# Performance work log

Hardware: AMD Instinct MI355X
Metric: run time of the kernel (lower is better)

The kernel has to match this reference:

```python
import jax, jax.numpy as jnp
import numpy as np

T, H, I, E, Z, TOPK = 1024, 1024, 512, 32, 8, 4
ROUTED_SCALING = 1.0


def setup_inputs() -> dict:
    key = jax.random.key(0)
    k1, k2, k3, k4 = jax.random.split(key, 4)
    return {
        "hidden_states": jax.random.normal(k1, (T, H), jnp.float32),
        "router_w": jax.random.normal(k2, (E + Z, H), jnp.float32) * 0.02,
        "correction_bias": jnp.zeros((E + Z,), jnp.float32),
        "w_gate_up": jax.random.normal(k3, (E, 2 * I, H), jnp.float32) * 0.02,
        "w_down": jax.random.normal(k4, (E, H, I), jnp.float32) * 0.02,
        "top_k": TOPK,
    }


def reference(hidden_states, router_w, correction_bias, w_gate_up, w_down, top_k):
    # hidden_states: [T, H]; router_w: [E+Z, H]; w_gate_up: [E, 2I, H]; w_down: [E, H, I]
    t, h = hidden_states.shape
    e = w_gate_up.shape[0]
    i = w_down.shape[2]
    # --- router (float32, no bias; correction bias only affects selection) ---
    logits = jnp.einsum("th,eh->te", hidden_states.astype(jnp.float32), router_w)
    scores = jax.nn.softmax(logits, axis=-1)                     # [T, E+Z]
    _, idx = jax.lax.top_k(scores + correction_bias[None, :], top_k)  # [T, k]
    w = jnp.take_along_axis(scores, idx, axis=1) * ROUTED_SCALING     # renormalize=False
    # combine matrix [T, E+Z] (sparse top-k scattered dense)
    comb = jnp.zeros((t, scores.shape[1]), jnp.float32)
    comb = comb.at[jnp.arange(t)[:, None], idx].add(w)
    comb_routed = comb[:, :e].astype(hidden_states.dtype)        # [T, E]
    zero_w = comb[:, e:].sum(-1).astype(hidden_states.dtype)     # [T] identity zero-experts
    # --- grouped SiLU-gated expert MLPs (dense all-experts reference) ---
    gu = jnp.einsum("th,eih->eti", hidden_states, w_gate_up)     # [E, T, 2I]
    hmid = jax.nn.silu(gu[..., :i]) * gu[..., i:]                # [E, T, I]
    ye = jnp.einsum("eti,ehi->eth", hmid, w_down)                # [E, T, H]
    out = jnp.einsum("te,eth->th", comb_routed, ye)
    out = out + zero_w[:, None] * hidden_states
    return out
```

## Files before the change

kernel.cpp:

```cpp
#include <hip/hip_runtime.h>
#include <hip/hip_bf16.h>
#include <math.h>

#define TT   1024
#define HH   1024
#define II   512
#define EE   32
#define NE   40
#define TOPK 4
#define CAP  1024

typedef __attribute__((ext_vector_type(4))) short short4v;
typedef __attribute__((ext_vector_type(8))) short short8v;
typedef __attribute__((ext_vector_type(4))) float floatx4;

static __device__ __forceinline__ short f2bf(float f) {
    unsigned u = __float_as_uint(f);
    unsigned r = (u + 0x7fffu + ((u >> 16) & 1u)) >> 16;
    return (short)(r & 0xffffu);
}
static __device__ __forceinline__ float bf2f(short s) {
    return __uint_as_float(((unsigned)(unsigned short)s) << 16);
}

#if defined(__has_builtin)
#if __has_builtin(__builtin_amdgcn_cvt_pk_bf16_f32)
#define HAVE_PK_BF16 1
#endif
#endif

static __device__ __forceinline__ unsigned pk2(float a, float b) {
#ifdef HAVE_PK_BF16
    typedef __attribute__((ext_vector_type(2))) __bf16 bf2t;
    union { bf2t v; unsigned u; } cv;
    cv.v = __builtin_amdgcn_cvt_pk_bf16_f32(a, b);
    return cv.u;
#else
    return (unsigned)(unsigned short)f2bf(a) | ((unsigned)(unsigned short)f2bf(b) << 16);
#endif
}
static __device__ __forceinline__ short4v cvt4(float4 v) {
    union { unsigned u[2]; short4v s; } cv;
    cv.u[0] = pk2(v.x, v.y); cv.u[1] = pk2(v.z, v.w);
    return cv.s;
}

#define WS_NEED_COMBINE 14942208ull

__global__ __launch_bounds__(256) void xconv_kernel(
    const float* __restrict__ x, short* __restrict__ xb)
{
    size_t i = ((size_t)blockIdx.x * 256 + threadIdx.x) * 8;
    float4 a = *(const float4*)&x[i];
    float4 b = *(const float4*)&x[i + 4];
    union { unsigned u[4]; short8v s; } cv;
    cv.u[0] = pk2(a.x, a.y); cv.u[1] = pk2(a.z, a.w);
    cv.u[2] = pk2(b.x, b.y); cv.u[3] = pk2(b.z, b.w);
    *(short8v*)&xb[i] = cv.s;
}

__global__ __launch_bounds__(64) void router_kernel(
    const float* __restrict__ x, const float* __restrict__ rw,
    const float* __restrict__ bias,
    float* __restrict__ topk_w, float* __restrict__ zero_w,
    int* __restrict__ kexp, int* __restrict__ counts, int* __restrict__ slots)
{
    const int t0 = blockIdx.x * 2;
    const int lane = threadIdx.x;

    float xv0[16], xv1[16];
    #pragma unroll
    for (int i = 0; i < 16; ++i) {
        xv0[i] = x[(size_t)t0 * HH + 64 * i + lane];
        xv1[i] = x[(size_t)(t0 + 1) * HH + 64 * i + lane];
    }

    float lg[2] = { -INFINITY, -INFINITY };
    for (int e0 = 0; e0 < NE; e0 += 4) {
        const float* r0 = rw + (size_t)e0 * HH;
        float p0[4] = {}, p1[4] = {};
        #pragma unroll
        for (int i = 0; i < 16; ++i) {
            int h = 64 * i + lane;
            float r[4];
            #pragma unroll
            for (int j = 0; j < 4; ++j) r[j] = r0[(size_t)j * HH + h];
            #pragma unroll
            for (int j = 0; j < 4; ++j) {
                p0[j] += xv0[i] * r[j];
                p1[j] += xv1[i] * r[j];
            }
        }
        #pragma unroll
        for (int j = 0; j < 4; ++j) {
            #pragma unroll
            for (int off = 32; off > 0; off >>= 1) {
                p0[j] += __shfl_xor(p0[j], off);
                p1[j] += __shfl_xor(p1[j], off);
            }
            if (lane == e0 + j) { lg[0] = p0[j]; lg[1] = p1[j]; }
        }
    }

    for (int j = 0; j < 2; ++j) {
        const int t = t0 + j;
        float ml = lg[j];
        float m = ml;
        #pragma unroll
        for (int off = 32; off > 0; off >>= 1) m = fmaxf(m, __shfl_xor(m, off));
        float pexp = (lane < NE) ? expf(ml - m) : 0.f;
        float s = pexp;
        #pragma unroll
        for (int off = 32; off > 0; off >>= 1) s += __shfl_xor(s, off);
        const float score = pexp / s;

        float val = (lane < NE) ? score + bias[lane] : -INFINITY;
        int   kidx[TOPK];
        float kw[TOPK];
        #pragma unroll
        for (int k = 0; k < TOPK; ++k) {
            float v = val; int idx = lane;
            #pragma unroll
            for (int off = 32; off > 0; off >>= 1) {
                float ov = __shfl_xor(v, off);
                int   oi = __shfl_xor(idx, off);
                if (ov > v || (ov == v && oi < idx)) { v = ov; idx = oi; }
            }
            kidx[k] = idx;
            kw[k]   = __shfl(score, idx);
            if (lane == idx) val = -INFINITY;
        }

        if (lane == 0) {
            float zw = 0.f;
            #pragma unroll
            for (int k = 0; k < TOPK; ++k) {
                int slot = t * TOPK + k;
                topk_w[slot] = kw[k];
                kexp[slot]   = kidx[k];
                if (kidx[k] < EE) {
                    int pos = atomicAdd(&counts[kidx[k]], 1);
                    slots[kidx[k] * CAP + pos] = slot;
                } else {
                    zw += kw[k];
                }
            }
            zero_w[t] = zw;
        }
    }
}

#define GM  128
#define GNP 32
#define GK  32
#define KP  40

__global__ __launch_bounds__(256) void gate_up_kernel(
    const short* __restrict__ xb, const float* __restrict__ wgu,
    const int* __restrict__ counts, const int* __restrict__ slots,
    const float* __restrict__ topk_w, short* __restrict__ hmid)
{
    const int e = blockIdx.y;
    const int cnt = counts[e];
    const int m_base = blockIdx.z * GM;
    if (m_base >= cnt) return;
    const int c_base = blockIdx.x * GNP;

    __shared__ short As[2][GM * KP];
    __shared__ short Bs[2][2 * GNP * KP];
    __shared__ int   sl[GM];
    __shared__ float wvs[GM];

    const int tid = threadIdx.x;
    if (tid < GM) {
        int m = m_base + tid;
        int s = (m < cnt) ? slots[e * CAP + m] : -1;
        sl[tid]  = s;
        wvs[tid] = (s >= 0) ? topk_w[s] : 0.f;
    }
    __syncthreads();

    const float* wb = wgu + (size_t)e * (2 * II) * HH;

    const int kcA = tid & 3;
    int rowA[2]; int slA[2]; const short* pA[2];
    #pragma unroll
    for (int it = 0; it < 2; ++it) {
        rowA[it] = (tid >> 2) + 64 * it;
        int s = sl[rowA[it]];
        slA[it] = s;
        pA[it] = xb + (size_t)((s >= 0 ? s : 0) >> 2) * HH + kcA * 8;
    }
    const int kq = tid & 7;
    int rowB[2]; const float* pB[2];
    #pragma unroll
    for (int it = 0; it < 2; ++it) {
        rowB[it] = (tid >> 3) + 32 * it;
        int grow = (rowB[it] < GNP) ? (c_base + rowB[it]) : (II + c_base + rowB[it] - GNP);
        pB[it] = wb + (size_t)grow * HH + kq * 4;
    }

    const int lane = tid & 63;
    const int wv_  = tid >> 6;
    const int wy   = wv_ & 1;
    const int wx   = wv_ >> 1;
    const int quad = lane >> 4;
    const int mcol = lane & 15;

    floatx4 accg[4] = {};
    floatx4 accu[4] = {};

    short8v pa[2]; float4 pb[2];
    const short8v sz = { 0,0,0,0,0,0,0,0 };

    #pragma unroll
    for (int it = 0; it < 2; ++it) pa[it] = (slA[it] >= 0) ? *(const short8v*)(pA[it]) : sz;
    #pragma unroll
    for (int it = 0; it < 2; ++it) pb[it] = *(const float4*)(pB[it]);
    #pragma unroll
    for (int it = 0; it < 2; ++it) *(short8v*)&As[0][rowA[it] * KP + kcA * 8] = pa[it];
    #pragma unroll
    for (int it = 0; it < 2; ++it) *(short4v*)&Bs[0][rowB[it] * KP + kq * 4] = cvt4(pb[it]);
    __syncthreads();

    int p = 0;
    for (int k0 = 0; k0 < HH; k0 += GK) {
        const int kn = k0 + GK;
        const bool more = kn < HH;
        if (more) {
            #pragma unroll
            for (int it = 0; it < 2; ++it) pa[it] = (slA[it] >= 0) ? *(const short8v*)(pA[it] + kn) : sz;
            #pragma unroll
            for (int it = 0; it < 2; ++it) pb[it] = *(const float4*)(pB[it] + kn);
        }

        short8v a[4], bg, bu;
        #pragma unroll
        for (int i = 0; i < 4; ++i)
            a[i] = *(const short8v*)&As[p][(wy * 64 + i * 16 + mcol) * KP + quad * 8];
        bg = *(const short8v*)&Bs[p][(wx * 16 + mcol) * KP + quad * 8];
        bu = *(const short8v*)&Bs[p][(GNP + wx * 16 + mcol) * KP + quad * 8];
        #pragma unroll
        for (int i = 0; i < 4; ++i) {
            accg[i] = __builtin_amdgcn_mfma_f32_16x16x32_bf16(a[i], bg, accg[i], 0, 0, 0);
            accu[i] = __builtin_amdgcn_mfma_f32_16x16x32_bf16(a[i], bu, accu[i], 0, 0, 0);
        }

        if (more) {
            #pragma unroll
            for (int it = 0; it < 2; ++it) *(short8v*)&As[1 - p][rowA[it] * KP + kcA * 8] = pa[it];
            #pragma unroll
            for (int it = 0; it < 2; ++it) *(short4v*)&Bs[1 - p][rowB[it] * KP + kq * 4] = cvt4(pb[it]);
        }
        __syncthreads();
        p ^= 1;
    }

    #pragma unroll
    for (int i = 0; i < 4; ++i) {
        #pragma unroll
        for (int r = 0; r < 4; ++r) {
            int m = wy * 64 + i * 16 + quad * 4 + r;
            int s = sl[m];
            if (s < 0) continue;
            float g = accg[i][r], u = accu[i][r];
            float valf = wvs[m] * g * u / (1.f + __expf(-g));
            hmid[(size_t)s * II + c_base + wx * 16 + mcol] = f2bf(valf);
        }
    }
}

#define DM 128
#define DN 64

template<int WRITE_Y>
__global__ __launch_bounds__(256) void down_kernel_t(
    const short* __restrict__ hmid, const float* __restrict__ wd,
    const int* __restrict__ counts, const int* __restrict__ slots,
    short* __restrict__ ydown, float* __restrict__ out)
{
    const int e = blockIdx.y;
    const int cnt = counts[e];
    const int m_base = blockIdx.z * DM;
    if (m_base >= cnt) return;
    const int n_base = blockIdx.x * DN;

    __shared__ short As[2][DM * KP];
    __shared__ short Bs[2][DN * KP];
    __shared__ int   sl[DM];

    const int tid = threadIdx.x;
    if (tid < DM) {
        int m = m_base + tid;
        sl[tid] = (m < cnt) ? slots[e * CAP + m] : -1;
    }
    __syncthreads();

    const float* wb = wd + (size_t)e * HH * II;

    const int kcA = tid & 3;
    int rowA[2]; int slA[2]; const short* pA[2];
    #pragma unroll
    for (int it = 0; it < 2; ++it) {
        rowA[it] = (tid >> 2) + 64 * it;
        int s = sl[rowA[it]];
        slA[it] = s;
        pA[it] = hmid + (size_t)(s >= 0 ? s : 0) * II + kcA * 8;
    }
    const int kq = tid & 7;
    int rowB[2]; const float* pB[2];
    #pragma unroll
    for (int it = 0; it < 2; ++it) {
        rowB[it] = (tid >> 3) + 32 * it;
        pB[it] = wb + (size_t)(n_base + rowB[it]) * II + kq * 4;
    }

    const int lane = tid & 63;
    const int wv_  = tid >> 6;
    const int wy   = wv_ & 1;
    const int wx   = wv_ >> 1;
    const int quad = lane >> 4;
    const int mcol = lane & 15;

    floatx4 acc[4][2] = {};

    short8v pa[2]; float4 pb[2];
    const short8v sz = { 0,0,0,0,0,0,0,0 };

    #pragma unroll
    for (int it = 0; it < 2; ++it) pa[it] = (slA[it] >= 0) ? *(const short8v*)(pA[it]) : sz;
    #pragma unroll
    for (int it = 0; it < 2; ++it) pb[it] = *(const float4*)(pB[it]);
    #pragma unroll
    for (int it = 0; it < 2; ++it) *(short8v*)&As[0][rowA[it] * KP + kcA * 8] = pa[it];
    #pragma unroll
    for (int it = 0; it < 2; ++it) *(short4v*)&Bs[0][rowB[it] * KP + kq * 4] = cvt4(pb[it]);
    __syncthreads();

    int p = 0;
    for (int k0 = 0; k0 < II; k0 += GK) {
        const int kn = k0 + GK;
        const bool more = kn < II;
        if (more) {
            #pragma unroll
            for (int it = 0; it < 2; ++it) pa[it] = (slA[it] >= 0) ? *(const short8v*)(pA[it] + kn) : sz;
            #pragma unroll
            for (int it = 0; it < 2; ++it) pb[it] = *(const float4*)(pB[it] + kn);
        }

        short8v a[4], b[2];
        #pragma unroll
        for (int i = 0; i < 4; ++i)
            a[i] = *(const short8v*)&As[p][(wy * 64 + i * 16 + mcol) * KP + quad * 8];
        #pragma unroll
        for (int j = 0; j < 2; ++j)
            b[j] = *(const short8v*)&Bs[p][(wx * 32 + j * 16 + mcol) * KP + quad * 8];
        #pragma unroll
        for (int i = 0; i < 4; ++i)
            #pragma unroll
            for (int j = 0; j < 2; ++j)
                acc[i][j] = __builtin_amdgcn_mfma_f32_16x16x32_bf16(a[i], b[j], acc[i][j], 0, 0, 0);

        if (more) {
            #pragma unroll
            for (int it = 0; it < 2; ++it) *(short8v*)&As[1 - p][rowA[it] * KP + kcA * 8] = pa[it];
            #pragma unroll
            for (int it = 0; it < 2; ++it) *(short4v*)&Bs[1 - p][rowB[it] * KP + kq * 4] = cvt4(pb[it]);
        }
        __syncthreads();
        p ^= 1;
    }

    #pragma unroll
    for (int i = 0; i < 4; ++i) {
        #pragma unroll
        for (int r = 0; r < 4; ++r) {
            int m = wy * 64 + i * 16 + quad * 4 + r;
            int s = sl[m];
            if (s < 0) continue;
            if (WRITE_Y) {
                short* yrow = ydown + (size_t)s * HH + n_base + wx * 32;
                #pragma unroll
                for (int j = 0; j < 2; ++j)
                    yrow[j * 16 + mcol] = f2bf(acc[i][j][r]);
            } else {
                float* orow = out + (size_t)(s >> 2) * HH + n_base + wx * 32;
                #pragma unroll
                for (int j = 0; j < 2; ++j)
                    atomicAdd(&orow[j * 16 + mcol], acc[i][j][r]);
            }
        }
    }
}

__global__ __launch_bounds__(256) void combine_kernel(
    const float* __restrict__ x, const short* __restrict__ ydown,
    const int* __restrict__ kexp, const float* __restrict__ zero_w,
    float* __restrict__ out)
{
    const int t = blockIdx.x;
    const int c = threadIdx.x;
    const float4 xv = ((const float4*)(x + (size_t)t * HH))[c];
    const float zw = zero_w[t];
    float4 o;
    o.x = zw * xv.x; o.y = zw * xv.y; o.z = zw * xv.z; o.w = zw * xv.w;
    #pragma unroll
    for (int k = 0; k < TOPK; ++k) {
        int slot = t * TOPK + k;
        if (kexp[slot] < EE) {
            short4v y = *(const short4v*)&ydown[(size_t)slot * HH + c * 4];
            o.x += bf2f(y[0]); o.y += bf2f(y[1]);
            o.z += bf2f(y[2]); o.w += bf2f(y[3]);
        }
    }
    ((float4*)(out + (size_t)t * HH))[c] = o;
}

__global__ __launch_bounds__(256) void zero_resid_kernel(
    const float* __restrict__ x, const float* __restrict__ zero_w,
    float* __restrict__ out)
{
    const int t = blockIdx.x;
    const float zw = zero_w[t];
    const int tid = threadIdx.x;
    const float4 xv = ((const float4*)(x + (size_t)t * HH))[tid];
    float4* o = (float4*)(out + (size_t)t * HH);
    float4 ov = o[tid];
    ov.x += zw * xv.x; ov.y += zw * xv.y; ov.z += zw * xv.z; ov.w += zw * xv.w;
    o[tid] = ov;
}

extern "C" void kernel_launch(void* const* d_in, const int* in_sizes, int n_in,
                              void* d_out, int out_size, void* d_ws, size_t ws_size,
                              hipStream_t stream) {
    const float* x    = (const float*)d_in[0];
    const float* rw   = (const float*)d_in[1];
    const float* bias = (const float*)d_in[2];
    const float* wgu  = (const float*)d_in[3];
    const float* wd   = (const float*)d_in[4];
    float* out = (float*)d_out;

    char* ws = (char*)d_ws;
    int*   counts = (int*)ws;
    float* topk_w = (float*)(ws + 1024);
    float* zero_w = (float*)(ws + 17408);
    int*   kexp   = (int*)(ws + 21504);
    int*   slots  = (int*)(ws + 40960);
    short* xb     = (short*)(ws + 262144);
    short* hmid   = (short*)(ws + 2359296);
    short* ydown  = (short*)(ws + 6553600);

    const bool big = ws_size >= WS_NEED_COMBINE;

    hipMemsetAsync(counts, 0, EE * sizeof(int), stream);
    if (!big) hipMemsetAsync(out, 0, (size_t)out_size * sizeof(float), stream);

    xconv_kernel<<<dim3(TT * HH / (256 * 8)), dim3(256), 0, stream>>>(x, xb);
    router_kernel<<<dim3(TT / 2), dim3(64), 0, stream>>>(
        x, rw, bias, topk_w, zero_w, kexp, counts, slots);
    gate_up_kernel<<<dim3(II / GNP, EE, CAP / GM), dim3(256), 0, stream>>>(
        xb, wgu, counts, slots, topk_w, hmid);
    if (big) {
        down_kernel_t<1><<<dim3(HH / DN, EE, CAP / DM), dim3(256), 0, stream>>>(
            hmid, wd, counts, slots, ydown, out);
        combine_kernel<<<dim3(TT), dim3(256), 0, stream>>>(
            x, ydown, kexp, zero_w, out);
    } else {
        down_kernel_t<0><<<dim3(HH / DN, EE, CAP / DM), dim3(256), 0, stream>>>(
            hmid, wd, counts, slots, nullptr, out);
        zero_resid_kernel<<<dim3(TT), dim3(256), 0, stream>>>(x, zero_w, out);
    }
}
```

Baseline: 331.1 us.

## Fuse MoE stages into one persistent cooperative kernel with grid syncs

Replaces the five separate launches (convert, router, gate-up, down, combine) with one cooperative kernel of 512 blocks that runs four phases separated by grid-wide syncs. Each block now owns one expert and column tile and loops over all token tiles, instead of launching a block per token tile. Shared-memory tiles drop from double to single buffering, and the router uses one wave per token with the bf16 conversion done by the other waves. The aim is to remove launch gaps and idle blocks for empty tiles. In exchange, load balance depends on per-expert token counts, the grid syncs add their own cost, and losing double buffering may expose global-memory latency.

```diff
diff --git a/kernel.cpp b/kernel.cpp
--- a/kernel.cpp
+++ b/kernel.cpp
@@ -1,6 +1,9 @@
 #include <hip/hip_runtime.h>
+#include <hip/hip_cooperative_groups.h>
 #include <hip/hip_bf16.h>
 #include <math.h>
+
+namespace cg = cooperative_groups;
 
 #define TT   1024
 #define HH   1024
@@ -10,6 +13,12 @@
 #define TOPK 4
 #define CAP  1024
 
+#define GM  128
+#define GNP 32
+#define GK  32
+#define KP  40
+#define DN  64
+
 typedef __attribute__((ext_vector_type(4))) short short4v;
 typedef __attribute__((ext_vector_type(8))) short short8v;
 typedef __attribute__((ext_vector_type(4))) float floatx4;
@@ -22,13 +31,11 @@
 static __device__ __forceinline__ float bf2f(short s) {
     return __uint_as_float(((unsigned)(unsigned short)s) << 16);
 }
-
 #if defined(__has_builtin)
 #if __has_builtin(__builtin_amdgcn_cvt_pk_bf16_f32)
 #define HAVE_PK_BF16 1
 #endif
 #endif
-
 static __device__ __forceinline__ unsigned pk2(float a, float b) {
 #ifdef HAVE_PK_BF16
     typedef __attribute__((ext_vector_type(2))) __bf16 bf2t;
@@ -45,70 +52,53 @@
     return cv.s;
 }
 
-#define WS_NEED_COMBINE 14942208ull
-
-__global__ __launch_bounds__(256) void xconv_kernel(
-    const float* __restrict__ x, short* __restrict__ xb)
-{
-    size_t i = ((size_t)blockIdx.x * 256 + threadIdx.x) * 8;
-    float4 a = *(const float4*)&x[i];
-    float4 b = *(const float4*)&x[i + 4];
-    union { unsigned u[4]; short8v s; } cv;
-    cv.u[0] = pk2(a.x, a.y); cv.u[1] = pk2(a.z, a.w);
-    cv.u[2] = pk2(b.x, b.y); cv.u[3] = pk2(b.z, b.w);
-    *(short8v*)&xb[i] = cv.s;
-}
-
-__global__ __launch_bounds__(64) void router_kernel(
+struct SMem {
+    short As[GM * KP];
+    short Bs[2 * GNP * KP];
+    int   sl[GM];
+    float wvs[GM];
+};
+
+
+static __device__ __forceinline__ void phaseA(
+    const int bx, const int tid,
     const float* __restrict__ x, const float* __restrict__ rw,
     const float* __restrict__ bias,
     float* __restrict__ topk_w, float* __restrict__ zero_w,
-    int* __restrict__ kexp, int* __restrict__ counts, int* __restrict__ slots)
-{
-    const int t0 = blockIdx.x * 2;
-    const int lane = threadIdx.x;
-
-    float xv0[16], xv1[16];
-    #pragma unroll
-    for (int i = 0; i < 16; ++i) {
-        xv0[i] = x[(size_t)t0 * HH + 64 * i + lane];
-        xv1[i] = x[(size_t)(t0 + 1) * HH + 64 * i + lane];
-    }
-
-    float lg[2] = { -INFINITY, -INFINITY };
-    for (int e0 = 0; e0 < NE; e0 += 4) {
-        const float* r0 = rw + (size_t)e0 * HH;
-        float p0[4] = {}, p1[4] = {};
-        #pragma unroll
-        for (int i = 0; i < 16; ++i) {
-            int h = 64 * i + lane;
-            float r[4];
-            #pragma unroll
-            for (int j = 0; j < 4; ++j) r[j] = r0[(size_t)j * HH + h];
+    int* __restrict__ kexp, int* __restrict__ counts,
+    int* __restrict__ slots, short* __restrict__ xb)
+{
+    const int lane = tid & 63;
+    const int w    = tid >> 6;
+
+    if (w < 2) {
+        const int t = bx * 2 + w;
+        float xv[16];
+        #pragma unroll
+        for (int i = 0; i < 16; ++i) xv[i] = x[(size_t)t * HH + 64 * i + lane];
+
+        float mylogit = -INFINITY;
+        for (int e0 = 0; e0 < NE; e0 += 4) {
+            const float* r0 = rw + (size_t)e0 * HH;
+            float p[4] = { 0.f, 0.f, 0.f, 0.f };
+            #pragma unroll
+            for (int i = 0; i < 16; ++i) {
+                int h = 64 * i + lane;
+                #pragma unroll
+                for (int j = 0; j < 4; ++j) p[j] += xv[i] * r0[(size_t)j * HH + h];
+            }
             #pragma unroll
             for (int j = 0; j < 4; ++j) {
-                p0[j] += xv0[i] * r[j];
-                p1[j] += xv1[i] * r[j];
-            }
-        }
-        #pragma unroll
-        for (int j = 0; j < 4; ++j) {
-            #pragma unroll
-            for (int off = 32; off > 0; off >>= 1) {
-                p0[j] += __shfl_xor(p0[j], off);
-                p1[j] += __shfl_xor(p1[j], off);
-            }
-            if (lane == e0 + j) { lg[0] = p0[j]; lg[1] = p1[j]; }
-        }
-    }
-
-    for (int j = 0; j < 2; ++j) {
-        const int t = t0 + j;
-        float ml = lg[j];
-        float m = ml;
+                #pragma unroll
+                for (int off = 32; off > 0; off >>= 1) p[j] += __shfl_xor(p[j], off);
+                if (lane == e0 + j) mylogit = p[j];
+            }
+        }
+
+        float m = mylogit;
         #pragma unroll
         for (int off = 32; off > 0; off >>= 1) m = fmaxf(m, __shfl_xor(m, off));
-        float pexp = (lane < NE) ? expf(ml - m) : 0.f;
+        float pexp = (lane < NE) ? expf(mylogit - m) : 0.f;
         float s = pexp;
         #pragma unroll
         for (int off = 32; off > 0; off >>= 1) s += __shfl_xor(s, off);
@@ -147,287 +137,292 @@
             }
             zero_w[t] = zw;
         }
-    }
-}
-
-#define GM  128
-#define GNP 32
-#define GK  32
-#define KP  40
-
-__global__ __launch_bounds__(256) void gate_up_kernel(
+    } else {
+        const int t = bx * 2 + (w - 2);
+        const float4* xr = (const float4*)(x + (size_t)t * HH);
+        short4v* xbr = (short4v*)(xb + (size_t)t * HH);
+        #pragma unroll
+        for (int i = 0; i < 4; ++i) xbr[lane + 64 * i] = cvt4(xr[lane + 64 * i]);
+    }
+}
+
+static __device__ __forceinline__ void phaseB(
+    const int bx, const int tid, SMem* sm,
     const short* __restrict__ xb, const float* __restrict__ wgu,
     const int* __restrict__ counts, const int* __restrict__ slots,
     const float* __restrict__ topk_w, short* __restrict__ hmid)
 {
-    const int e = blockIdx.y;
-    const int cnt = counts[e];
-    const int m_base = blockIdx.z * GM;
-    if (m_base >= cnt) return;
-    const int c_base = blockIdx.x * GNP;
-
-    __shared__ short As[2][GM * KP];
-    __shared__ short Bs[2][2 * GNP * KP];
-    __shared__ int   sl[GM];
-    __shared__ float wvs[GM];
-
-    const int tid = threadIdx.x;
-    if (tid < GM) {
-        int m = m_base + tid;
-        int s = (m < cnt) ? slots[e * CAP + m] : -1;
-        sl[tid]  = s;
-        wvs[tid] = (s >= 0) ? topk_w[s] : 0.f;
-    }
-    __syncthreads();
-
-    const float* wb = wgu + (size_t)e * (2 * II) * HH;
-
-    const int kcA = tid & 3;
-    int rowA[2]; int slA[2]; const short* pA[2];
-    #pragma unroll
-    for (int it = 0; it < 2; ++it) {
-        rowA[it] = (tid >> 2) + 64 * it;
-        int s = sl[rowA[it]];
-        slA[it] = s;
-        pA[it] = xb + (size_t)((s >= 0 ? s : 0) >> 2) * HH + kcA * 8;
-    }
-    const int kq = tid & 7;
-    int rowB[2]; const float* pB[2];
-    #pragma unroll
-    for (int it = 0; it < 2; ++it) {
-        rowB[it] = (tid >> 3) + 32 * it;
-        int grow = (rowB[it] < GNP) ? (c_base + rowB[it]) : (II + c_base + rowB[it] - GNP);
-        pB[it] = wb + (size_t)grow * HH + kq * 4;
-    }
+    const int e      = bx >> 4;
+    const int c_base = (bx & 15) * GNP;
+    const int cnt    = counts[e];
+    const float* wb  = wgu + (size_t)e * (2 * II) * HH;
 
     const int lane = tid & 63;
-    const int wv_  = tid >> 6;
-    const int wy   = wv_ & 1;
-    const int wx   = wv_ >> 1;
+    const int w    = tid >> 6;
+    const int wy   = w & 1;
+    const int wx   = w >> 1;
     const int quad = lane >> 4;
     const int mcol = lane & 15;
 
-    floatx4 accg[4] = {};
-    floatx4 accu[4] = {};
-
-    short8v pa[2]; float4 pb[2];
-    const short8v sz = { 0,0,0,0,0,0,0,0 };
-
-    #pragma unroll
-    for (int it = 0; it < 2; ++it) pa[it] = (slA[it] >= 0) ? *(const short8v*)(pA[it]) : sz;
-    #pragma unroll
-    for (int it = 0; it < 2; ++it) pb[it] = *(const float4*)(pB[it]);
-    #pragma unroll
-    for (int it = 0; it < 2; ++it) *(short8v*)&As[0][rowA[it] * KP + kcA * 8] = pa[it];
-    #pragma unroll
-    for (int it = 0; it < 2; ++it) *(short4v*)&Bs[0][rowB[it] * KP + kq * 4] = cvt4(pb[it]);
-    __syncthreads();
-
-    int p = 0;
-    for (int k0 = 0; k0 < HH; k0 += GK) {
-        const int kn = k0 + GK;
-        const bool more = kn < HH;
-        if (more) {
-            #pragma unroll
-            for (int it = 0; it < 2; ++it) pa[it] = (slA[it] >= 0) ? *(const short8v*)(pA[it] + kn) : sz;
-            #pragma unroll
-            for (int it = 0; it < 2; ++it) pb[it] = *(const float4*)(pB[it] + kn);
-        }
-
-        short8v a[4], bg, bu;
-        #pragma unroll
-        for (int i = 0; i < 4; ++i)
-            a[i] = *(const short8v*)&As[p][(wy * 64 + i * 16 + mcol) * KP + quad * 8];
-        bg = *(const short8v*)&Bs[p][(wx * 16 + mcol) * KP + quad * 8];
-        bu = *(const short8v*)&Bs[p][(GNP + wx * 16 + mcol) * KP + quad * 8];
+    for (int m_base = 0; m_base < cnt; m_base += GM) {
+        if (tid < GM) {
+            int m = m_base + tid;
+            int s = (m < cnt) ? slots[e * CAP + m] : -1;
+            sm->sl[tid]  = s;
+            sm->wvs[tid] = (s >= 0) ? topk_w[s] : 0.f;
+        }
+        __syncthreads();
+
+        const int kcA = tid & 3;
+        int rowA[2]; int slA[2]; const short* pA[2];
+        #pragma unroll
+        for (int it = 0; it < 2; ++it) {
+            rowA[it] = (tid >> 2) + 64 * it;
+            int s = sm->sl[rowA[it]];
+            slA[it] = s;
+            pA[it] = xb + (size_t)((s >= 0 ? s : 0) >> 2) * HH + kcA * 8;
+        }
+        const int kq = tid & 7;
+        int rowB[2]; const float* pB[2];
+        #pragma unroll
+        for (int it = 0; it < 2; ++it) {
+            rowB[it] = (tid >> 3) + 32 * it;
+            int grow = (rowB[it] < GNP) ? (c_base + rowB[it])
+                                        : (II + c_base + rowB[it] - GNP);
+            pB[it] = wb + (size_t)grow * HH + kq * 4;
+        }
+
+        floatx4 accg[4] = {};
+        floatx4 accu[4] = {};
+        short8v pa[2]; float4 pb[2];
+        const short8v szv = { 0,0,0,0,0,0,0,0 };
+
+        #pragma unroll
+        for (int it = 0; it < 2; ++it) pa[it] = (slA[it] >= 0) ? *(const short8v*)(pA[it]) : szv;
+        #pragma unroll
+        for (int it = 0; it < 2; ++it) pb[it] = *(const float4*)(pB[it]);
+
+        for (int k0 = 0; k0 < HH; k0 += GK) {
+            #pragma unroll
+            for (int it = 0; it < 2; ++it) *(short8v*)&sm->As[rowA[it] * KP + kcA * 8] = pa[it];
+            #pragma unroll
+            for (int it = 0; it < 2; ++it) *(short4v*)&sm->Bs[rowB[it] * KP + kq * 4] = cvt4(pb[it]);
+            __syncthreads();
+
+            const int kn = k0 + GK;
+            if (kn < HH) {
+                #pragma unroll
+                for (int it = 0; it < 2; ++it) pa[it] = (slA[it] >= 0) ? *(const short8v*)(pA[it] + kn) : szv;
+                #pragma unroll
+                for (int it = 0; it < 2; ++it) pb[it] = *(const float4*)(pB[it] + kn);
+            }
+
+            short8v a[4], bg, bu;
+            #pragma unroll
+            for (int i = 0; i < 4; ++i)
+                a[i] = *(const short8v*)&sm->As[(wy * 64 + i * 16 + mcol) * KP + quad * 8];
+            bg = *(const short8v*)&sm->Bs[(wx * 16 + mcol) * KP + quad * 8];
+            bu = *(const short8v*)&sm->Bs[(GNP + wx * 16 + mcol) * KP + quad * 8];
+            #pragma unroll
+            for (int i = 0; i < 4; ++i) {
+                accg[i] = __builtin_amdgcn_mfma_f32_16x16x32_bf16(a[i], bg, accg[i], 0, 0, 0);
+                accu[i] = __builtin_amdgcn_mfma_f32_16x16x32_bf16(a[i], bu, accu[i], 0, 0, 0);
+            }
+            __syncthreads();
+        }
+
         #pragma unroll
         for (int i = 0; i < 4; ++i) {
-            accg[i] = __builtin_amdgcn_mfma_f32_16x16x32_bf16(a[i], bg, accg[i], 0, 0, 0);
-            accu[i] = __builtin_amdgcn_mfma_f32_16x16x32_bf16(a[i], bu, accu[i], 0, 0, 0);
-        }
-
-        if (more) {
-            #pragma unroll
-            for (int it = 0; it < 2; ++it) *(short8v*)&As[1 - p][rowA[it] * KP + kcA * 8] = pa[it];
-            #pragma unroll
-            for (int it = 0; it < 2; ++it) *(short4v*)&Bs[1 - p][rowB[it] * KP + kq * 4] = cvt4(pb[it]);
+            #pragma unroll
+            for (int r = 0; r < 4; ++r) {
+                int m = wy * 64 + i * 16 + quad * 4 + r;
+                int s = sm->sl[m];
+                if (s < 0) continue;
+                float g = accg[i][r], u = accu[i][r];
+                float valf = sm->wvs[m] * g * u / (1.f + __expf(-g));
+                hmid[(size_t)s * II + c_base + wx * 16 + mcol] = f2bf(valf);
+            }
         }
         __syncthreads();
-        p ^= 1;
-    }
-
-    #pragma unroll
-    for (int i = 0; i < 4; ++i) {
-        #pragma unroll
-        for (int r = 0; r < 4; ++r) {
-            int m = wy * 64 + i * 16 + quad * 4 + r;
-            int s = sl[m];
-            if (s < 0) continue;
-            float g = accg[i][r], u = accu[i][r];
-            float valf = wvs[m] * g * u / (1.f + __expf(-g));
-            hmid[(size_t)s * II + c_base + wx * 16 + mcol] = f2bf(valf);
-        }
-    }
-}
-
-#define DM 128
-#define DN 64
-
-template<int WRITE_Y>
-__global__ __launch_bounds__(256) void down_kernel_t(
+    }
+}
+
+static __device__ __forceinline__ void phaseC(
+    const int bx, const int tid, SMem* sm,
     const short* __restrict__ hmid, const float* __restrict__ wd,
     const int* __restrict__ counts, const int* __restrict__ slots,
-    short* __restrict__ ydown, float* __restrict__ out)
-{
-    const int e = blockIdx.y;
-    const int cnt = counts[e];
-    const int m_base = blockIdx.z * DM;
-    if (m_base >= cnt) return;
-    const int n_base = blockIdx.x * DN;
-
-    __shared__ short As[2][DM * KP];
-    __shared__ short Bs[2][DN * KP];
-    __shared__ int   sl[DM];
-
-    const int tid = threadIdx.x;
-    if (tid < DM) {
-        int m = m_base + tid;
-        sl[tid] = (m < cnt) ? slots[e * CAP + m] : -1;
-    }
-    __syncthreads();
-
-    const float* wb = wd + (size_t)e * HH * II;
-
-    const int kcA = tid & 3;
-    int rowA[2]; int slA[2]; const short* pA[2];
-    #pragma unroll
-    for (int it = 0; it < 2; ++it) {
-        rowA[it] = (tid >> 2) + 64 * it;
-        int s = sl[rowA[it]];
-        slA[it] = s;
-        pA[it] = hmid + (size_t)(s >= 0 ? s : 0) * II + kcA * 8;
-    }
-    const int kq = tid & 7;
-    int rowB[2]; const float* pB[2];
-    #pragma unroll
-    for (int it = 0; it < 2; ++it) {
-        rowB[it] = (tid >> 3) + 32 * it;
-        pB[it] = wb + (size_t)(n_base + rowB[it]) * II + kq * 4;
-    }
+    short* __restrict__ ydown)
+{
+    const int e      = bx >> 4;
+    const int n_base = (bx & 15) * DN;
+    const int cnt    = counts[e];
+    const float* wb  = wd + (size_t)e * HH * II;
 
     const int lane = tid & 63;
-    const int wv_  = tid >> 6;
-    const int wy   = wv_ & 1;
-    const int wx   = wv_ >> 1;
+    const int w    = tid >> 6;
+    const int wy   = w & 1;
+    const int wx   = w >> 1;
     const int quad = lane >> 4;
     const int mcol = lane & 15;
 
-    floatx4 acc[4][2] = {};
-
-    short8v pa[2]; float4 pb[2];
-    const short8v sz = { 0,0,0,0,0,0,0,0 };
-
-    #pragma unroll
-    for (int it = 0; it < 2; ++it) pa[it] = (slA[it] >= 0) ? *(const short8v*)(pA[it]) : sz;
-    #pragma unroll
-    for (int it = 0; it < 2; ++it) pb[it] = *(const float4*)(pB[it]);
-    #pragma unroll
-    for (int it = 0; it < 2; ++it) *(short8v*)&As[0][rowA[it] * KP + kcA * 8] = pa[it];
-    #pragma unroll
-    for (int it = 0; it < 2; ++it) *(short4v*)&Bs[0][rowB[it] * KP + kq * 4] = cvt4(pb[it]);
-    __syncthreads();
-
-    int p = 0;
-    for (int k0 = 0; k0 < II; k0 += GK) {
-        const int kn = k0 + GK;
-        const bool more = kn < II;
-        if (more) {
-            #pragma unroll
-            for (int it = 0; it < 2; ++it) pa[it] = (slA[it] >= 0) ? *(const short8v*)(pA[it] + kn) : sz;
-            #pragma unroll
-            for (int it = 0; it < 2; ++it) pb[it] = *(const float4*)(pB[it] + kn);
-        }
-
-        short8v a[4], b[2];
-        #pragma unroll
-        for (int i = 0; i < 4; ++i)
-            a[i] = *(const short8v*)&As[p][(wy * 64 + i * 16 + mcol) * KP + quad * 8];
-        #pragma unroll
-        for (int j = 0; j < 2; ++j)
-            b[j] = *(const short8v*)&Bs[p][(wx * 32 + j * 16 + mcol) * KP + quad * 8];
-        #pragma unroll
-        for (int i = 0; i < 4; ++i)
+    for (int m_base = 0; m_base < cnt; m_base += GM) {
+        if (tid < GM) {
+            int m = m_base + tid;
+            sm->sl[tid] = (m < cnt) ? slots[e * CAP + m] : -1;
+        }
+        __syncthreads();
+
+        const int kcA = tid & 3;
+        int rowA[2]; int slA[2]; const short* pA[2];
+        #pragma unroll
+        for (int it = 0; it < 2; ++it) {
+            rowA[it] = (tid >> 2) + 64 * it;
+            int s = sm->sl[rowA[it]];
+            slA[it] = s;
+            pA[it] = hmid + (size_t)(s >= 0 ? s : 0) * II + kcA * 8;
+        }
+        const int kq = tid & 7;
+        int rowB[2]; const float* pB[2];
+        #pragma unroll
+        for (int it = 0; it < 2; ++it) {
+            rowB[it] = (tid >> 3) + 32 * it;
+            pB[it] = wb + (size_t)(n_base + rowB[it]) * II + kq * 4;
+        }
+
+        floatx4 acc[4][2] = {};
+        short8v pa[2]; float4 pb[2];
+        const short8v szv = { 0,0,0,0,0,0,0,0 };
+
+        #pragma unroll
+        for (int it = 0; it < 2; ++it) pa[it] = (slA[it] >= 0) ? *(const short8v*)(pA[it]) : szv;
+        #pragma unroll
+        for (int it = 0; it < 2; ++it) pb[it] = *(const float4*)(pB[it]);
+
+        for (int k0 = 0; k0 < II; k0 += GK) {
+            #pragma unroll
+            for (int it = 0; it < 2; ++it) *(short8v*)&sm->As[rowA[it] * KP + kcA * 8] = pa[it];
+            #pragma unroll
+            for (int it = 0; it < 2; ++it) *(short4v*)&sm->Bs[rowB[it] * KP + kq * 4] = cvt4(pb[it]);
+            __syncthreads();
+
+            const int kn = k0 + GK;
+            if (kn < II) {
+                #pragma unroll
+                for (int it = 0; it < 2; ++it) pa[it] = (slA[it] >= 0) ? *(const short8v*)(pA[it] + kn) : szv;
+                #pragma unroll
+                for (int it = 0; it < 2; ++it) pb[it] = *(const float4*)(pB[it] + kn);
+            }
+
+            short8v a[4], b[2];
+            #pragma unroll
+            for (int i = 0; i < 4; ++i)
+                a[i] = *(const short8v*)&sm->As[(wy * 64 + i * 16 + mcol) * KP + quad * 8];
             #pragma unroll
             for (int j = 0; j < 2; ++j)
-                acc[i][j] = __builtin_amdgcn_mfma_f32_16x16x32_bf16(a[i], b[j], acc[i][j], 0, 0, 0);
-
-        if (more) {
-            #pragma unroll
-            for (int it = 0; it < 2; ++it) *(short8v*)&As[1 - p][rowA[it] * KP + kcA * 8] = pa[it];
-            #pragma unroll
-            for (int it = 0; it < 2; ++it) *(short4v*)&Bs[1 - p][rowB[it] * KP + kq * 4] = cvt4(pb[it]);
-        }
-        __syncthreads();
-        p ^= 1;
-    }
-
-    #pragma unroll
-    for (int i = 0; i < 4; ++i) {
-        #pragma unroll
-        for (int r = 0; r < 4; ++r) {
-            int m = wy * 64 + i * 16 + quad * 4 + r;
-            int s = sl[m];
-            if (s < 0) continue;
-            if (WRITE_Y) {
+                b[j] = *(const short8v*)&sm->Bs[(wx * 32 + j * 16 + mcol) * KP + quad * 8];
+            #pragma unroll
+            for (int i = 0; i < 4; ++i)
+                #pragma unroll
+                for (int j = 0; j < 2; ++j)
+                    acc[i][j] = __builtin_amdgcn_mfma_f32_16x16x32_bf16(a[i], b[j], acc[i][j], 0, 0, 0);
+            __syncthreads();
+        }
+
+        #pragma unroll
+        for (int i = 0; i < 4; ++i) {
+            #pragma unroll
+            for (int r = 0; r < 4; ++r) {
+                int m = wy * 64 + i * 16 + quad * 4 + r;
+                int s = sm->sl[m];
+                if (s < 0) continue;
                 short* yrow = ydown + (size_t)s * HH + n_base + wx * 32;
                 #pragma unroll
                 for (int j = 0; j < 2; ++j)
                     yrow[j * 16 + mcol] = f2bf(acc[i][j][r]);
-            } else {
-                float* orow = out + (size_t)(s >> 2) * HH + n_base + wx * 32;
-                #pragma unroll
-                for (int j = 0; j < 2; ++j)
-                    atomicAdd(&orow[j * 16 + mcol], acc[i][j][r]);
-            }
-        }
-    }
-}
-
-__global__ __launch_bounds__(256) void combine_kernel(
+            }
+        }
+        __syncthreads();
+    }
+}
+
+static __device__ __forceinline__ void phaseD(
+    const int bx, const int tid,
     const float* __restrict__ x, const short* __restrict__ ydown,
     const int* __restrict__ kexp, const float* __restrict__ zero_w,
     float* __restrict__ out)
 {
-    const int t = blockIdx.x;
-    const int c = threadIdx.x;
-    const float4 xv = ((const float4*)(x + (size_t)t * HH))[c];
-    const float zw = zero_w[t];
-    float4 o;
-    o.x = zw * xv.x; o.y = zw * xv.y; o.z = zw * xv.z; o.w = zw * xv.w;
     #pragma unroll
-    for (int k = 0; k < TOPK; ++k) {
-        int slot = t * TOPK + k;
-        if (kexp[slot] < EE) {
-            short4v y = *(const short4v*)&ydown[(size_t)slot * HH + c * 4];
-            o.x += bf2f(y[0]); o.y += bf2f(y[1]);
-            o.z += bf2f(y[2]); o.w += bf2f(y[3]);
-        }
-    }
-    ((float4*)(out + (size_t)t * HH))[c] = o;
-}
-
-__global__ __launch_bounds__(256) void zero_resid_kernel(
-    const float* __restrict__ x, const float* __restrict__ zero_w,
+    for (int j = 0; j < 2; ++j) {
+        const int t = bx * 2 + j;
+        const float4 xvv = ((const float4*)(x + (size_t)t * HH))[tid];
+        const float zw = zero_w[t];
+        float4 o;
+        o.x = zw * xvv.x; o.y = zw * xvv.y; o.z = zw * xvv.z; o.w = zw * xvv.w;
+        #pragma unroll
+        for (int k = 0; k < TOPK; ++k) {
+            int slot = t * TOPK + k;
+            if (kexp[slot] < EE) {
+                short4v y = *(const short4v*)&ydown[(size_t)slot * HH + tid * 4];
+                o.x += bf2f(y[0]); o.y += bf2f(y[1]);
+                o.z += bf2f(y[2]); o.w += bf2f(y[3]);
+            }
+        }
+        ((float4*)(out + (size_t)t * HH))[tid] = o;
+    }
+}
+
+__global__ __launch_bounds__(256, 2) void fused_moe(
+    const float* __restrict__ x, const float* __restrict__ rw,
+    const float* __restrict__ bias, const float* __restrict__ wgu,
+    const float* __restrict__ wd, float* __restrict__ out,
+    int* __restrict__ counts, float* __restrict__ topk_w,
+    float* __restrict__ zero_w, int* __restrict__ kexp,
+    int* __restrict__ slots, short* __restrict__ xb,
+    short* __restrict__ hmid, short* __restrict__ ydown)
+{
+    cg::grid_group grid = cg::this_grid();
+    __shared__ SMem sm;
+    const int bx = blockIdx.x, tid = threadIdx.x;
+
+    phaseA(bx, tid, x, rw, bias, topk_w, zero_w, kexp, counts, slots, xb);
+    __threadfence(); grid.sync();
+    phaseB(bx, tid, &sm, xb, wgu, counts, slots, topk_w, hmid);
+    __threadfence(); grid.sync();
+    phaseC(bx, tid, &sm, hmid, wd, counts, slots, ydown);
+    __threadfence(); grid.sync();
+    phaseD(bx, tid, x, ydown, kexp, zero_w, out);
+}
+
+__global__ __launch_bounds__(256, 2) void kA(
+    const float* __restrict__ x, const float* __restrict__ rw,
+    const float* __restrict__ bias, float* __restrict__ topk_w,
+    float* __restrict__ zero_w, int* __restrict__ kexp,
+    int* __restrict__ counts, int* __restrict__ slots, short* __restrict__ xb)
+{
+    phaseA(blockIdx.x, threadIdx.x, x, rw, bias, topk_w, zero_w, kexp, counts, slots, xb);
+}
+__global__ __launch_bounds__(256, 2) void kB(
+    const short* __restrict__ xb, const float* __restrict__ wgu,
+    const int* __restrict__ counts, const int* __restrict__ slots,
+    const float* __restrict__ topk_w, short* __restrict__ hmid)
+{
+    __shared__ SMem sm;
+    phaseB(blockIdx.x, threadIdx.x, &sm, xb, wgu, counts, slots, topk_w, hmid);
+}
+__global__ __launch_bounds__(256, 2) void kC(
+    const short* __restrict__ hmid, const float* __restrict__ wd,
+    const int* __restrict__ counts, const int* __restrict__ slots,
+    short* __restrict__ ydown)
+{
+    __shared__ SMem sm;
+    phaseC(blockIdx.x, threadIdx.x, &sm, hmid, wd, counts, slots, ydown);
+}
+__global__ __launch_bounds__(256, 2) void kD(
+    const float* __restrict__ x, const short* __restrict__ ydown,
+    const int* __restrict__ kexp, const float* __restrict__ zero_w,
     float* __restrict__ out)
 {
-    const int t = blockIdx.x;
-    const float zw = zero_w[t];
-    const int tid = threadIdx.x;
-    const float4 xv = ((const float4*)(x + (size_t)t * HH))[tid];
-    float4* o = (float4*)(out + (size_t)t * HH);
-    float4 ov = o[tid];
-    ov.x += zw * xv.x; ov.y += zw * xv.y; ov.z += zw * xv.z; ov.w += zw * xv.w;
-    o[tid] = ov;
+    phaseD(blockIdx.x, threadIdx.x, x, ydown, kexp, zero_w, out);
 }
 
 extern "C" void kernel_launch(void* const* d_in, const int* in_sizes, int n_in,
@@ -450,24 +445,26 @@
     short* hmid   = (short*)(ws + 2359296);
     short* ydown  = (short*)(ws + 6553600);
 
-    const bool big = ws_size >= WS_NEED_COMBINE;
-
     hipMemsetAsync(counts, 0, EE * sizeof(int), stream);
-    if (!big) hipMemsetAsync(out, 0, (size_t)out_size * sizeof(float), stream);
-
-    xconv_kernel<<<dim3(TT * HH / (256 * 8)), dim3(256), 0, stream>>>(x, xb);
-    router_kernel<<<dim3(TT / 2), dim3(64), 0, stream>>>(
-        x, rw, bias, topk_w, zero_w, kexp, counts, slots);
-    gate_up_kernel<<<dim3(II / GNP, EE, CAP / GM), dim3(256), 0, stream>>>(
-        xb, wgu, counts, slots, topk_w, hmid);
-    if (big) {
-        down_kernel_t<1><<<dim3(HH / DN, EE, CAP / DM), dim3(256), 0, stream>>>(
-            hmid, wd, counts, slots, ydown, out);
-        combine_kernel<<<dim3(TT), dim3(256), 0, stream>>>(
-            x, ydown, kexp, zero_w, out);
-    } else {
-        down_kernel_t<0><<<dim3(HH / DN, EE, CAP / DM), dim3(256), 0, stream>>>(
-            hmid, wd, counts, slots, nullptr, out);
-        zero_resid_kernel<<<dim3(TT), dim3(256), 0, stream>>>(x, zero_w, out);
-    }
-}
+
+    int nb = 0;
+    hipError_t qerr = hipOccupancyMaxActiveBlocksPerMultiprocessor(&nb, fused_moe, 256, 0);
+    bool launched = false;
+    if (qerr == hipSuccess && nb >= 2) {
+        void* args[] = {
+            (void*)&x, (void*)&rw, (void*)&bias, (void*)&wgu, (void*)&wd,
+            (void*)&out, (void*)&counts, (void*)&topk_w, (void*)&zero_w,
+            (void*)&kexp, (void*)&slots, (void*)&xb, (void*)&hmid, (void*)&ydown
+        };
+        hipError_t lerr = hipLaunchCooperativeKernel((const void*)fused_moe,
+                                                     dim3(512), dim3(256),
+                                                     args, 0, stream);
+        launched = (lerr == hipSuccess);
+    }
+    if (!launched) {
+        kA<<<dim3(512), dim3(256), 0, stream>>>(x, rw, bias, topk_w, zero_w, kexp, counts, slots, xb);
+        kB<<<dim3(512), dim3(256), 0, stream>>>(xb, wgu, counts, slots, topk_w, hmid);
+        kC<<<dim3(512), dim3(256), 0, stream>>>(hmid, wd, counts, slots, ydown);
+        kD<<<dim3(512), dim3(256), 0, stream>>>(x, ydown, kexp, zero_w, out);
+    }
+}
```

Result: faster. 311.3 us (-6.0%).
